# Kernel optimization log

Measured on AMD Instinct MI355X. Metric: run time of the kernel, lower is better.

## Reference

```python
import jax, jax.numpy as jnp
import numpy as np

EMBED_DIM = 1024
NUM_HEADS = 16
HEAD_DIM = EMBED_DIM // NUM_HEADS


def setup_inputs() -> dict:
    key = jax.random.key(0)
    ks = jax.random.split(key, 6)
    s = 1.0 / np.sqrt(EMBED_DIM)
    x = jax.random.normal(ks[0], (2, 2048, EMBED_DIM), dtype=jnp.float32)
    Wk = jax.random.uniform(ks[1], (EMBED_DIM, EMBED_DIM), jnp.float32, -s, s)
    Wq = jax.random.uniform(ks[2], (EMBED_DIM, EMBED_DIM), jnp.float32, -s, s)
    Wv = jax.random.uniform(ks[3], (EMBED_DIM, EMBED_DIM), jnp.float32, -s, s)
    Wo = jax.random.uniform(ks[4], (EMBED_DIM, EMBED_DIM), jnp.float32, -s, s)
    bo = jax.random.uniform(ks[5], (EMBED_DIM,), jnp.float32, -s, s)
    return {"x": x, "Wq": Wq, "Wk": Wk, "Wv": Wv, "Wo": Wo, "bo": bo}


def reference(x, Wq, Wk, Wv, Wo, bo):
    b, s, e = x.shape
    h, d = NUM_HEADS, HEAD_DIM
    scale = d ** (-0.5)
    # nn.Linear: y = x @ W.T ; here W stored as [out, in] -> use W.T
    q = (x @ Wq.T).reshape(b, s, h, d).transpose(0, 2, 1, 3)  # b h s d
    k = (x @ Wk.T).reshape(b, s, h, d).transpose(0, 2, 1, 3)
    v = (x @ Wv.T).reshape(b, s, h, d).transpose(0, 2, 1, 3)
    logits = jnp.einsum('bhqd,bhkd->bhqk', q, k) * scale
    attn = jax.nn.softmax(logits, axis=-1)
    out = jnp.einsum('bhqk,bhkd->bhqd', attn, v)
    out = out.transpose(0, 2, 1, 3).reshape(b, s, e)
    return out @ Wo.T + bo
```

## Files before the change

kernel.cpp:

```cpp
#include <hip/hip_runtime.h>
#include <hip/hip_bf16.h>

using short8 = __attribute__((ext_vector_type(8))) short;
using f32x4  = __attribute__((ext_vector_type(4))) float;
using uint4v = __attribute__((ext_vector_type(4))) unsigned;

#if __has_builtin(__builtin_amdgcn_exp2f)
#define EXP2(x) __builtin_amdgcn_exp2f(x)
#else
#define EXP2(x) exp2f(x)
#endif

__device__ __forceinline__ short f2bf(float f) {
    union { float f; unsigned u; } v; v.f = f;
    unsigned r = v.u + 0x7fffu + ((v.u >> 16) & 1u);
    return (short)(r >> 16);
}
__device__ __forceinline__ unsigned pack_trunc(float a, float b) {
    union { float f; unsigned u; } ua, ub; ua.f = a; ub.f = b;
#if __has_builtin(__builtin_amdgcn_perm)
    return __builtin_amdgcn_perm(ub.u, ua.u, 0x07060302u);
#else
    return (ub.u & 0xFFFF0000u) | (ua.u >> 16);
#endif
}
__device__ __forceinline__ void async_copy16(const short* g, short* s) {
    __builtin_amdgcn_global_load_lds(
        (const __attribute__((address_space(1))) void*)g,
        (__attribute__((address_space(3))) void*)s, 16, 0, 0);
}

__global__ __launch_bounds__(256) void cvt_f32_bf16(
    const float* __restrict__ s0, const float* __restrict__ s1,
    const float* __restrict__ s2, const float* __restrict__ s3,
    const float* __restrict__ s4,
    short* __restrict__ d0, short* __restrict__ d1, short* __restrict__ d2,
    short* __restrict__ d3, short* __restrict__ d4,
    int n0, int n1, int n2, int n3, int n4) {
    const float* s; short* d; int n;
    switch (blockIdx.y) {
        case 0: s = s0; d = d0; n = n0; break;
        case 1: s = s1; d = d1; n = n1; break;
        case 2: s = s2; d = d2; n = n2; break;
        case 3: s = s3; d = d3; n = n3; break;
        default: s = s4; d = d4; n = n4; break;
    }
    const int idx = (blockIdx.x * 256 + threadIdx.x) * 4;
    if (idx < n) {
        float4 v = *(const float4*)(s + idx);
        short4 o;
        o.x = f2bf(v.x); o.y = f2bf(v.y); o.z = f2bf(v.z); o.w = f2bf(v.w);
        *(short4*)(d + idx) = o;
    }
}

template <int MODE>
__device__ __forceinline__ void gemm_body(const short* __restrict__ A,
                                          const short* __restrict__ B,
                                          short* __restrict__ C,
                                          float scale) {
    constexpr int Kd = 1024, Nd = 1024, Sd = 2048;
    __shared__ __align__(16) short As[128 * 32];
    __shared__ __align__(16) short Bs[128 * 32];

    const int tid  = threadIdx.x;
    const int w    = tid >> 6, lane = tid & 63;
    const int quad = lane >> 4, l16 = lane & 15;
    const int wm   = (w >> 1) * 64, wn = (w & 1) * 64;
    const int bm   = blockIdx.y * 128, bn = blockIdx.x * 128;

    f32x4 acc[4][4];
#pragma unroll
    for (int i = 0; i < 4; ++i)
#pragma unroll
        for (int j = 0; j < 4; ++j) acc[i][j] = (f32x4){0.f, 0.f, 0.f, 0.f};

    for (int k0 = 0; k0 < Kd; k0 += 32) {
        __syncthreads();
#pragma unroll
        for (int c = 0; c < 2; ++c) {
            int li  = c * 256 + tid;
            int row = li >> 2;
            int col = (li & 3) * 8;
            async_copy16(A + (size_t)(bm + row) * Kd + k0 + col, &As[li * 8]);
            async_copy16(B + (size_t)(bn + row) * Kd + k0 + col, &Bs[li * 8]);
        }
        __syncthreads();

        short8 af[4], bfv[4];
#pragma unroll
        for (int mi = 0; mi < 4; ++mi)
            af[mi] = *(const short8*)(&As[(wm + mi * 16 + l16) * 32 + quad * 8]);
#pragma unroll
        for (int ni = 0; ni < 4; ++ni)
            bfv[ni] = *(const short8*)(&Bs[(wn + ni * 16 + l16) * 32 + quad * 8]);
#pragma unroll
        for (int mi = 0; mi < 4; ++mi)
#pragma unroll
            for (int ni = 0; ni < 4; ++ni) {
                if constexpr (MODE == 2)
                    acc[mi][ni] = __builtin_amdgcn_mfma_f32_16x16x32_bf16(
                        bfv[ni], af[mi], acc[mi][ni], 0, 0, 0);
                else
                    acc[mi][ni] = __builtin_amdgcn_mfma_f32_16x16x32_bf16(
                        af[mi], bfv[ni], acc[mi][ni], 0, 0, 0);
            }
    }

    if constexpr (MODE == 2) {
#pragma unroll
        for (int mi = 0; mi < 4; ++mi) {
            const int m_g = bm + wm + mi * 16 + l16;
            const int b_  = m_g >> 11, s_ = m_g & 2047;
#pragma unroll
            for (int ni = 0; ni < 4; ++ni)
#pragma unroll
                for (int r = 0; r < 4; ++r) {
                    const int n_g = bn + wn + ni * 16 + quad * 4 + r;
                    C[(size_t)b_ * Nd * Sd + (size_t)n_g * Sd + s_] =
                        f2bf(acc[mi][ni][r]);
                }
        }
    } else {
#pragma unroll
        for (int ni = 0; ni < 4; ++ni) {
            const int colg = bn + wn + ni * 16 + l16;
#pragma unroll
            for (int mi = 0; mi < 4; ++mi)
#pragma unroll
                for (int r = 0; r < 4; ++r) {
                    const int rowg = bm + wm + mi * 16 + quad * 4 + r;
                    C[(size_t)rowg * Nd + colg] = f2bf(acc[mi][ni][r] * scale);
                }
        }
    }
}

#define CSC 0.18033688f

__global__ __launch_bounds__(256, 2) void proj_gemm(
    const short* __restrict__ X,
    const short* __restrict__ Wq, const short* __restrict__ Wk,
    const short* __restrict__ Wv,
    short* __restrict__ Qo, short* __restrict__ Ko, short* __restrict__ VTo) {
    if (blockIdx.z == 0)
        gemm_body<0>(X, Wq, Qo, CSC);
    else if (blockIdx.z == 1)
        gemm_body<0>(X, Wk, Ko, 1.0f);
    else
        gemm_body<2>(X, Wv, VTo, 1.0f);
}

__global__ __launch_bounds__(256, 2) void out_gemm(
    const short* __restrict__ A, const short* __restrict__ B,
    const float* __restrict__ bias, float* __restrict__ C) {
    constexpr int Kd = 1024, Nd = 1024;
    __shared__ __align__(16) short As[64 * 32];
    __shared__ __align__(16) short Bs[128 * 32];

    const int tid  = threadIdx.x;
    const int w    = tid >> 6, lane = tid & 63;
    const int quad = lane >> 4, l16 = lane & 15;
    const int wm   = (w >> 1) * 32, wn = (w & 1) * 64;
    const int bm   = blockIdx.y * 64, bn = blockIdx.x * 128;

    f32x4 acc[2][4];
#pragma unroll
    for (int i = 0; i < 2; ++i)
#pragma unroll
        for (int j = 0; j < 4; ++j) acc[i][j] = (f32x4){0.f, 0.f, 0.f, 0.f};

    for (int k0 = 0; k0 < Kd; k0 += 32) {
        __syncthreads();
        {
            int row = tid >> 2, col = (tid & 3) * 8;
            async_copy16(A + (size_t)(bm + row) * Kd + k0 + col, &As[tid * 8]);
        }
#pragma unroll
        for (int c = 0; c < 2; ++c) {
            int li  = c * 256 + tid;
            int row = li >> 2;
            int col = (li & 3) * 8;
            async_copy16(B + (size_t)(bn + row) * Kd + k0 + col, &Bs[li * 8]);
        }
        __syncthreads();

        short8 af[2], bfv[4];
#pragma unroll
        for (int mi = 0; mi < 2; ++mi)
            af[mi] = *(const short8*)(&As[(wm + mi * 16 + l16) * 32 + quad * 8]);
#pragma unroll
        for (int ni = 0; ni < 4; ++ni)
            bfv[ni] = *(const short8*)(&Bs[(wn + ni * 16 + l16) * 32 + quad * 8]);
#pragma unroll
        for (int mi = 0; mi < 2; ++mi)
#pragma unroll
            for (int ni = 0; ni < 4; ++ni)
                acc[mi][ni] = __builtin_amdgcn_mfma_f32_16x16x32_bf16(
                    af[mi], bfv[ni], acc[mi][ni], 0, 0, 0);
    }

#pragma unroll
    for (int ni = 0; ni < 4; ++ni) {
        const int colg = bn + wn + ni * 16 + l16;
        const float bv = bias[colg];
#pragma unroll
        for (int mi = 0; mi < 2; ++mi)
#pragma unroll
            for (int r = 0; r < 4; ++r) {
                const int rowg = bm + wm + mi * 16 + quad * 4 + r;
                C[(size_t)rowg * Nd + colg] = acc[mi][ni][r] + bv;
            }
    }
}

__global__ __launch_bounds__(128, 1) void attn_kernel(
    const short* __restrict__ Q, const short* __restrict__ K,
    const short* __restrict__ VT, short* __restrict__ O) {
    constexpr int S = 2048, E = 1024, NT = S / 64;
    __shared__ __align__(16) short Ks[2][64 * 64];
    __shared__ __align__(16) short Vs[2][64 * 64];

    const int tid  = threadIdx.x;
    const int w    = tid >> 6, lane = tid & 63;
    const int quad = lane >> 4, l16 = lane & 15;
    const int bh   = blockIdx.y, b = bh >> 4, h = bh & 15;
    const int qt   = blockIdx.x;

    const int    q0   = qt * 128 + w * 64;
    const size_t base = (size_t)b * S * E;
    const size_t vtb  = (size_t)b * E * S;
    const int    hc   = h * 64;
    const int    xr   = l16 & 7;

    short8 aq[4][2];
#pragma unroll
    for (int qg = 0; qg < 4; ++qg) {
        const short* qp = Q + base + (size_t)(q0 + qg * 16 + l16) * E + hc + quad * 8;
        aq[qg][0] = *(const short8*)(qp);
        aq[qg][1] = *(const short8*)(qp + 32);
    }

    f32x4 oT[4][4], o_sum[4];
#pragma unroll
    for (int qg = 0; qg < 4; ++qg) {
        o_sum[qg] = (f32x4){0.f, 0.f, 0.f, 0.f};
#pragma unroll
        for (int i = 0; i < 4; ++i) oT[qg][i] = (f32x4){0.f, 0.f, 0.f, 0.f};
    }

    int          kdst[4], vdst0[4], vdst1[4];
    const short* kga[4];
    const short* vga[4];
#pragma unroll
    for (int c = 0; c < 4; ++c) {
        int li = c * 128 + tid, row = li >> 3, cc = li & 7;
        kdst[c] = row * 64 + ((cc ^ (row & 7)) * 8);
        int c0   = 4 * (cc >> 2) + 2 * (cc & 1);
        int boff = 4 * ((cc >> 1) & 1);
        vdst0[c] = row * 64 + ((c0 ^ (row & 7)) * 8) + boff;
        vdst1[c] = row * 64 + (((c0 + 1) ^ (row & 7)) * 8) + boff;
        kga[c]   = K + base + (size_t)row * E + hc + cc * 8;
        vga[c]   = VT + vtb + (size_t)(hc + row) * S + cc * 8;
    }

    short8 kr[4], vr[4];
#pragma unroll
    for (int c = 0; c < 4; ++c) {
        kr[c] = *(const short8*)(kga[c]);
        vr[c] = *(const short8*)(vga[c]);
    }
#pragma unroll
    for (int c = 0; c < 4; ++c) {
        *(short8*)(&Ks[0][kdst[c]]) = kr[c];
        short4 lo, hi;
        lo.x = vr[c][0]; lo.y = vr[c][1]; lo.z = vr[c][2]; lo.w = vr[c][3];
        hi.x = vr[c][4]; hi.y = vr[c][5]; hi.z = vr[c][6]; hi.w = vr[c][7];
        *(short4*)(&Vs[0][vdst0[c]]) = lo;
        *(short4*)(&Vs[0][vdst1[c]]) = hi;
    }
#pragma unroll
    for (int c = 0; c < 4; ++c) {
        kr[c] = *(const short8*)(kga[c] + (size_t)64 * E);
        vr[c] = *(const short8*)(vga[c] + 64);
    }
    __syncthreads();

    const short8 ones = (short8){0x3F80, 0x3F80, 0x3F80, 0x3F80,
                                 0x3F80, 0x3F80, 0x3F80, 0x3F80};
    const float  LB   = 0.00281502f;

    for (int kt = 0; kt < NT; ++kt) {
        const int    cur = kt & 1;
        const short* Kc  = Ks[cur];
        const short* Vc  = Vs[cur];

        if (kt + 1 < NT) {
            short* Kn = Ks[cur ^ 1];
            short* Vn = Vs[cur ^ 1];
#pragma unroll
            for (int c = 0; c < 4; ++c) {
                *(short8*)(&Kn[kdst[c]]) = kr[c];
                short4 lo, hi;
                lo.x = vr[c][0]; lo.y = vr[c][1]; lo.z = vr[c][2]; lo.w = vr[c][3];
                hi.x = vr[c][4]; hi.y = vr[c][5]; hi.z = vr[c][6]; hi.w = vr[c][7];
                *(short4*)(&Vn[vdst0[c]]) = lo;
                *(short4*)(&Vn[vdst1[c]]) = hi;
            }
            if (kt + 2 < NT) {
#pragma unroll
                for (int c = 0; c < 4; ++c) {
                    kr[c] = *(const short8*)(kga[c] + (size_t)(kt + 2) * 64 * E);
                    vr[c] = *(const short8*)(vga[c] + (kt + 2) * 64);
                }
            }
        }

        uint4v pkv[4][2];
#pragma unroll
        for (int kn = 0; kn < 4; ++kn) {
            const short* kb  = &Kc[(kn * 16 + l16) * 64];
            short8       bk0 = *(const short8*)(kb + ((quad ^ xr) * 8));
            short8       bk1 = *(const short8*)(kb + (((quad + 4) ^ xr) * 8));
#pragma unroll
            for (int qg = 0; qg < 4; ++qg) {
                f32x4 a = (f32x4){LB, LB, LB, LB};
                a = __builtin_amdgcn_mfma_f32_16x16x32_bf16(bk0, aq[qg][0], a, 0, 0, 0);
                a = __builtin_amdgcn_mfma_f32_16x16x32_bf16(bk1, aq[qg][1], a, 0, 0, 0);
                pkv[qg][kn >> 1][(kn & 1) * 2]     = pack_trunc(EXP2(a[0]), EXP2(a[1]));
                pkv[qg][kn >> 1][(kn & 1) * 2 + 1] = pack_trunc(EXP2(a[2]), EXP2(a[3]));
            }
        }

#pragma unroll
        for (int ks = 0; ks < 2; ++ks) {
            short8 pf[4];
#pragma unroll
            for (int qg = 0; qg < 4; ++qg) {
                union { uint4v u; short8 s; } cv;
                cv.u   = pkv[qg][ks];
                pf[qg] = cv.s;
                o_sum[qg] = __builtin_amdgcn_mfma_f32_16x16x32_bf16(
                    ones, pf[qg], o_sum[qg], 0, 0, 0);
            }
#pragma unroll
            for (int ni = 0; ni < 4; ++ni) {
                const int rv = ni * 16 + l16;
                short8 vb =
                    *(const short8*)(&Vc[rv * 64 + (((ks * 4 + quad) ^ xr) * 8)]);
#pragma unroll
                for (int qg = 0; qg < 4; ++qg)
                    oT[qg][ni] = __builtin_amdgcn_mfma_f32_16x16x32_bf16(
                        vb, pf[qg], oT[qg][ni], 0, 0, 0);
            }
        }
        __syncthreads();
    }

#pragma unroll
    for (int qg = 0; qg < 4; ++qg) {
        const float inv = 1.0f / o_sum[qg][0];
        const int   qg_ = q0 + qg * 16 + l16;
#pragma unroll
        for (int ni = 0; ni < 4; ++ni) {
            short4 ov;
            ov.x = f2bf(oT[qg][ni][0] * inv);
            ov.y = f2bf(oT[qg][ni][1] * inv);
            ov.z = f2bf(oT[qg][ni][2] * inv);
            ov.w = f2bf(oT[qg][ni][3] * inv);
            *(short4*)(&O[base + (size_t)qg_ * E + hc + ni * 16 + quad * 4]) = ov;
        }
    }
}

extern "C" void kernel_launch(void* const* d_in, const int* in_sizes, int n_in,
                              void* d_out, int out_size, void* d_ws, size_t ws_size,
                              hipStream_t stream) {
    const float* x  = (const float*)d_in[0];
    const float* Wq = (const float*)d_in[1];
    const float* Wk = (const float*)d_in[2];
    const float* Wv = (const float*)d_in[3];
    const float* Wo = (const float*)d_in[4];
    const float* bo = (const float*)d_in[5];
    float* out = (float*)d_out;

    constexpr int XN = 2 * 2048 * 1024;
    constexpr int WN = 1024 * 1024;

    short* Xb  = (short*)d_ws;
    short* Wqb = Xb + XN;
    short* Wkb = Wqb + WN;
    short* Wvb = Wkb + WN;
    short* Wob = Wvb + WN;
    short* Qb  = Wob + WN;
    short* Kb  = Qb + XN;
    short* VTb = Kb + XN;

    cvt_f32_bf16<<<dim3(4096, 5), 256, 0, stream>>>(
        x, Wq, Wk, Wv, Wo, Xb, Wqb, Wkb, Wvb, Wob, XN, WN, WN, WN, WN);
    proj_gemm<<<dim3(8, 32, 3), 256, 0, stream>>>(Xb, Wqb, Wkb, Wvb, Qb, Kb, VTb);
    attn_kernel<<<dim3(16, 32), 128, 0, stream>>>(Qb, Kb, VTb, Xb );
    out_gemm<<<dim3(8, 64), 256, 0, stream>>>(Xb, Wob, bo, out);
}
```

Measured before the change: 191.5 us.

## Split key sequence across two thread groups per attention block and reduce

Doubles the attention block to 256 threads, with two 128-thread teams each handling half of the key/value sequence in separate shared-memory double buffers. At the end, one team writes its partial output accumulators and row sums to shared memory and the other adds them before normalizing and storing. This aims to raise the number of active waves per CU and shorten the serial key loop. It costs a larger shared-memory footprint and an extra reduction step with a barrier.

```diff
diff --git a/kernel.cpp b/kernel.cpp
--- a/kernel.cpp
+++ b/kernel.cpp
@@ -214,20 +214,24 @@
     }
 }
 
-__global__ __launch_bounds__(128, 1) void attn_kernel(
+__global__ __launch_bounds__(256, 2) void attn_kernel(
     const short* __restrict__ Q, const short* __restrict__ K,
     const short* __restrict__ VT, short* __restrict__ O) {
-    constexpr int S = 2048, E = 1024, NT = S / 64;
-    __shared__ __align__(16) short Ks[2][64 * 64];
-    __shared__ __align__(16) short Vs[2][64 * 64];
+    constexpr int S = 2048, E = 1024, NIT = 16;
+    __shared__ __align__(16) short smem[32768];
 
     const int tid  = threadIdx.x;
     const int w    = tid >> 6, lane = tid & 63;
     const int quad = lane >> 4, l16 = lane & 15;
     const int bh   = blockIdx.y, b = bh >> 4, h = bh & 15;
     const int qt   = blockIdx.x;
-
-    const int    q0   = qt * 128 + w * 64;
+    const int p    = w & 1;
+    const int t    = w >> 1;
+
+    short* const KsT = smem + t * 8192;
+    short* const VsT = smem + 16384 + t * 8192;
+
+    const int    q0   = qt * 128 + p * 64;
     const size_t base = (size_t)b * S * E;
     const size_t vtb  = (size_t)b * E * S;
     const int    hc   = h * 64;
@@ -249,19 +253,20 @@
         for (int i = 0; i < 4; ++i) oT[qg][i] = (f32x4){0.f, 0.f, 0.f, 0.f};
     }
 
+    const int    ttid = tid & 127;
     int          kdst[4], vdst0[4], vdst1[4];
     const short* kga[4];
     const short* vga[4];
 #pragma unroll
     for (int c = 0; c < 4; ++c) {
-        int li = c * 128 + tid, row = li >> 3, cc = li & 7;
+        int li = c * 128 + ttid, row = li >> 3, cc = li & 7;
         kdst[c] = row * 64 + ((cc ^ (row & 7)) * 8);
         int c0   = 4 * (cc >> 2) + 2 * (cc & 1);
         int boff = 4 * ((cc >> 1) & 1);
         vdst0[c] = row * 64 + ((c0 ^ (row & 7)) * 8) + boff;
         vdst1[c] = row * 64 + (((c0 + 1) ^ (row & 7)) * 8) + boff;
-        kga[c]   = K + base + (size_t)row * E + hc + cc * 8;
-        vga[c]   = VT + vtb + (size_t)(hc + row) * S + cc * 8;
+        kga[c]   = K + base + (size_t)(t * 1024 + row) * E + hc + cc * 8;
+        vga[c]   = VT + vtb + (size_t)(hc + row) * S + t * 1024 + cc * 8;
     }
 
     short8 kr[4], vr[4];
@@ -272,12 +277,12 @@
     }
 #pragma unroll
     for (int c = 0; c < 4; ++c) {
-        *(short8*)(&Ks[0][kdst[c]]) = kr[c];
+        *(short8*)(&KsT[kdst[c]]) = kr[c];
         short4 lo, hi;
         lo.x = vr[c][0]; lo.y = vr[c][1]; lo.z = vr[c][2]; lo.w = vr[c][3];
         hi.x = vr[c][4]; hi.y = vr[c][5]; hi.z = vr[c][6]; hi.w = vr[c][7];
-        *(short4*)(&Vs[0][vdst0[c]]) = lo;
-        *(short4*)(&Vs[0][vdst1[c]]) = hi;
+        *(short4*)(&VsT[vdst0[c]]) = lo;
+        *(short4*)(&VsT[vdst1[c]]) = hi;
     }
 #pragma unroll
     for (int c = 0; c < 4; ++c) {
@@ -290,14 +295,14 @@
                                  0x3F80, 0x3F80, 0x3F80, 0x3F80};
     const float  LB   = 0.00281502f;
 
-    for (int kt = 0; kt < NT; ++kt) {
+    for (int kt = 0; kt < NIT; ++kt) {
         const int    cur = kt & 1;
-        const short* Kc  = Ks[cur];
-        const short* Vc  = Vs[cur];
-
-        if (kt + 1 < NT) {
-            short* Kn = Ks[cur ^ 1];
-            short* Vn = Vs[cur ^ 1];
+        const short* Kc  = KsT + cur * 4096;
+        const short* Vc  = VsT + cur * 4096;
+
+        if (kt + 1 < NIT) {
+            short* Kn = KsT + (cur ^ 1) * 4096;
+            short* Vn = VsT + (cur ^ 1) * 4096;
 #pragma unroll
             for (int c = 0; c < 4; ++c) {
                 *(short8*)(&Kn[kdst[c]]) = kr[c];
@@ -307,7 +312,7 @@
                 *(short4*)(&Vn[vdst0[c]]) = lo;
                 *(short4*)(&Vn[vdst1[c]]) = hi;
             }
-            if (kt + 2 < NT) {
+            if (kt + 2 < NIT) {
 #pragma unroll
                 for (int c = 0; c < 4; ++c) {
                     kr[c] = *(const short8*)(kga[c] + (size_t)(kt + 2) * 64 * E);
@@ -357,18 +362,36 @@
         __syncthreads();
     }
 
-#pragma unroll
-    for (int qg = 0; qg < 4; ++qg) {
-        const float inv = 1.0f / o_sum[qg][0];
-        const int   qg_ = q0 + qg * 16 + l16;
-#pragma unroll
-        for (int ni = 0; ni < 4; ++ni) {
-            short4 ov;
-            ov.x = f2bf(oT[qg][ni][0] * inv);
-            ov.y = f2bf(oT[qg][ni][1] * inv);
-            ov.z = f2bf(oT[qg][ni][2] * inv);
-            ov.w = f2bf(oT[qg][ni][3] * inv);
-            *(short4*)(&O[base + (size_t)qg_ * E + hc + ni * 16 + quad * 4]) = ov;
+    float* red  = (float*)smem;
+    float* sum4 = red + 128 * 68;
+    if (t == 1) {
+        float* dst = red + (p * 64 + lane) * 68;
+#pragma unroll
+        for (int qg = 0; qg < 4; ++qg)
+#pragma unroll
+            for (int ni = 0; ni < 4; ++ni)
+                *(f32x4*)(dst + (qg * 4 + ni) * 4) = oT[qg][ni];
+        f32x4 s4 = (f32x4){o_sum[0][0], o_sum[1][0], o_sum[2][0], o_sum[3][0]};
+        *(f32x4*)(sum4 + (p * 64 + lane) * 4) = s4;
+    }
+    __syncthreads();
+    if (t == 0) {
+        const float* src = red + (p * 64 + lane) * 68;
+        f32x4 s4 = *(const f32x4*)(sum4 + (p * 64 + lane) * 4);
+#pragma unroll
+        for (int qg = 0; qg < 4; ++qg) {
+            const float inv = 1.0f / (o_sum[qg][0] + s4[qg]);
+            const int   qg_ = q0 + qg * 16 + l16;
+#pragma unroll
+            for (int ni = 0; ni < 4; ++ni) {
+                f32x4 o = oT[qg][ni] + *(const f32x4*)(src + (qg * 4 + ni) * 4);
+                short4 ov;
+                ov.x = f2bf(o[0] * inv);
+                ov.y = f2bf(o[1] * inv);
+                ov.z = f2bf(o[2] * inv);
+                ov.w = f2bf(o[3] * inv);
+                *(short4*)(&O[base + (size_t)qg_ * E + hc + ni * 16 + quad * 4]) = ov;
+            }
         }
     }
 }
@@ -399,6 +422,6 @@
     cvt_f32_bf16<<<dim3(4096, 5), 256, 0, stream>>>(
         x, Wq, Wk, Wv, Wo, Xb, Wqb, Wkb, Wvb, Wob, XN, WN, WN, WN, WN);
     proj_gemm<<<dim3(8, 32, 3), 256, 0, stream>>>(Xb, Wqb, Wkb, Wvb, Qb, Kb, VTb);
-    attn_kernel<<<dim3(16, 32), 128, 0, stream>>>(Qb, Kb, VTb, Xb );
+    attn_kernel<<<dim3(16, 32), 256, 0, stream>>>(Qb, Kb, VTb, Xb );
     out_gemm<<<dim3(8, 64), 256, 0, stream>>>(Xb, Wob, bo, out);
 }
```

Measured after the change: 178.9 us. 6.6% less time.
